# Kernel optimization log

Measured on AMD Instinct MI355X. Metric: run time of the kernel, lower is better.

Reference implementation:

```python
import jax, jax.numpy as jnp
import numpy as np

N_NODES = 100000
N_EDGES = 1600000
N_GRAPHS = 64
NEG_SLOPE = 0.2


def gat_conv(x, W, att_src, att_dst, bias, edge_index, n_nodes, heads, out_ch, concat):
    """PyG-style GATConv (eval mode, self loops already included in edge_index)."""
    h = (x @ W).reshape(n_nodes, heads, out_ch)            # [N, H, C]
    a_src = jnp.einsum('nhc,hc->nh', h, att_src)           # [N, H]
    a_dst = jnp.einsum('nhc,hc->nh', h, att_dst)           # [N, H]
    src, dst = edge_index[0], edge_index[1]
    e = jax.nn.leaky_relu(a_src[src] + a_dst[dst], NEG_SLOPE)   # [E, H]
    # segment softmax over incoming edges of each destination node
    m = jax.ops.segment_max(e, dst, num_segments=n_nodes)      # [N, H]
    ex = jnp.exp(e - m[dst])
    denom = jax.ops.segment_sum(ex, dst, num_segments=n_nodes) # [N, H]
    alpha = ex / denom[dst]                                     # [E, H]
    msg = h[src] * alpha[:, :, None]                            # [E, H, C]
    out = jax.ops.segment_sum(msg, dst, num_segments=n_nodes)   # [N, H, C]
    if concat:
        out = out.reshape(n_nodes, heads * out_ch)
    else:
        out = out.mean(axis=1)
    return out + bias


def setup_inputs() -> dict:
    key = jax.random.key(0)
    ks = jax.random.split(key, 16)
    x = jax.random.normal(ks[0], (N_NODES, 1), dtype=jnp.float32)
    edge_index = jax.random.randint(ks[1], (2, N_EDGES), 0, N_NODES, dtype=jnp.int64)
    batch = jnp.sort(jax.random.randint(ks[2], (N_NODES,), 0, N_GRAPHS, dtype=jnp.int64))
    def glorot(k, shape):
        fan = (shape[0] + shape[-1])
        return jax.random.uniform(k, shape, jnp.float32, -1.0, 1.0) * np.sqrt(6.0 / fan)
    # layer 1: in=1, heads=8, out=8, concat
    W1 = glorot(ks[3], (1, 64))
    att_src1 = glorot(ks[4], (8, 8))
    att_dst1 = glorot(ks[5], (8, 8))
    b1 = jnp.zeros((64,), jnp.float32)
    # layer 2: in=64, heads=8, out=16, mean
    W2 = glorot(ks[6], (64, 128))
    att_src2 = glorot(ks[7], (8, 16))
    att_dst2 = glorot(ks[8], (8, 16))
    b2 = jnp.zeros((16,), jnp.float32)
    # fc 16 -> 4
    Wfc = glorot(ks[9], (16, 4))
    bfc = jnp.zeros((4,), jnp.float32)
    return dict(x=x, W1=W1, att_src1=att_src1, att_dst1=att_dst1, b1=b1,
                W2=W2, att_src2=att_src2, att_dst2=att_dst2, b2=b2,
                Wfc=Wfc, bfc=bfc, edge_index=edge_index, batch=batch)


def reference(x, W1, att_src1, att_dst1, b1, W2, att_src2, att_dst2, b2, Wfc, bfc, edge_index, batch):
    n = x.shape[0]
    # PyG GATConv default add_self_loops=True
    loops = jnp.arange(n, dtype=edge_index.dtype)
    ei = jnp.concatenate([edge_index, jnp.stack([loops, loops])], axis=1)
    h = gat_conv(x, W1, att_src1, att_dst1, b1, ei, n, heads=8, out_ch=8, concat=True)
    h = jax.nn.elu(h)
    # F.dropout(training=False) and attention dropout are no-ops in eval mode
    h = gat_conv(h, W2, att_src2, att_dst2, b2, ei, n, heads=8, out_ch=16, concat=False)
    # global mean pool over graphs
    sums = jax.ops.segment_sum(h, batch, num_segments=N_GRAPHS)          # [G, 16]
    cnts = jax.ops.segment_sum(jnp.ones((n,), h.dtype), batch, num_segments=N_GRAPHS)
    pooled = sums / jnp.maximum(cnts, 1.0)[:, None]
    return pooled @ Wfc + bfc                                            # [G, 4]
```

## Files before the change

### kernel.cpp

```cpp
#include <hip/hip_runtime.h>
#include <hip/hip_fp16.h>

#define N_NODES  100000
#define N_EDGES  1600000
#define N_GRAPHS 64

#define BINSH  8
#define NBIN   392
#define BINCAP 5120
#define EPB    4096

typedef _Float16 half8 __attribute__((ext_vector_type(8)));
typedef float float4v __attribute__((ext_vector_type(4)));

__device__ __forceinline__ float lrelu(float v) { return v > 0.f ? v : 0.2f * v; }
__device__ __forceinline__ float elu_f(float v) { return v > 0.f ? v : __expf(v) - 1.f; }

__global__ __launch_bounds__(1024) void k_binA(
    const int* __restrict__ src, const int* __restrict__ dst,
    const int* __restrict__ batch, int* __restrict__ gbin_cursor,
    int* __restrict__ cnt, int* __restrict__ binned) {
    __shared__ int hist[NBIN], lexcl[NBIN], runbase[NBIN], lcur[NBIN];
    __shared__ int wpart[16];
    __shared__ int gh[N_GRAPHS];
    __shared__ int2 stage[EPB];
    int t = threadIdx.x;
    int e0 = blockIdx.x * EPB;
    for (int b = t; b < NBIN; b += 1024) hist[b] = 0;
    if (t < N_GRAPHS) gh[t] = 0;
    __syncthreads();
    int nid = blockIdx.x * 1024 + t;
    if (nid < N_NODES) atomicAdd(&gh[batch[nid]], 1);
    int e = 4 * t;
    int4 dv = make_int4(0, 0, 0, 0), sv = make_int4(0, 0, 0, 0);
    bool full = (e0 + e + 3 < N_EDGES);
    if (full) {
        dv = *(const int4*)(dst + e0 + e);
        sv = *(const int4*)(src + e0 + e);
        atomicAdd(&hist[dv.x >> BINSH], 1);
        atomicAdd(&hist[dv.y >> BINSH], 1);
        atomicAdd(&hist[dv.z >> BINSH], 1);
        atomicAdd(&hist[dv.w >> BINSH], 1);
    } else {
        for (int k = 0; k < 4; ++k)
            if (e0 + e + k < N_EDGES) atomicAdd(&hist[dst[e0 + e + k] >> BINSH], 1);
    }
    __syncthreads();
    int v = (t < NBIN) ? hist[t] : 0;
    int x = v;
#pragma unroll
    for (int d = 1; d < 64; d <<= 1) {
        int y = __shfl_up(x, d, 64);
        if ((t & 63) >= d) x += y;
    }
    if ((t & 63) == 63) wpart[t >> 6] = x;
    __syncthreads();
    if (t == 0) {
        int a = 0;
        for (int w = 0; w < 16; ++w) { int q = wpart[w]; wpart[w] = a; a += q; }
    }
    __syncthreads();
    int excl = x - v + wpart[t >> 6];
    if (t < NBIN) { lexcl[t] = excl; lcur[t] = excl; }
    __syncthreads();
    if (t < NBIN && v > 0) runbase[t] = atomicAdd(&gbin_cursor[t], v);
    if (t < N_GRAPHS && gh[t]) atomicAdd(&cnt[t], gh[t]);
    __syncthreads();
    if (full) {
        int p, b_;
        b_ = dv.x >> BINSH; p = atomicAdd(&lcur[b_], 1);
        stage[p] = make_int2(((dv.x & 255) << 17) | sv.x, b_);
        b_ = dv.y >> BINSH; p = atomicAdd(&lcur[b_], 1);
        stage[p] = make_int2(((dv.y & 255) << 17) | sv.y, b_);
        b_ = dv.z >> BINSH; p = atomicAdd(&lcur[b_], 1);
        stage[p] = make_int2(((dv.z & 255) << 17) | sv.z, b_);
        b_ = dv.w >> BINSH; p = atomicAdd(&lcur[b_], 1);
        stage[p] = make_int2(((dv.w & 255) << 17) | sv.w, b_);
    } else {
        for (int k = 0; k < 4; ++k) {
            if (e0 + e + k < N_EDGES) {
                int d = dst[e0 + e + k];
                int b_ = d >> BINSH;
                int p = atomicAdd(&lcur[b_], 1);
                stage[p] = make_int2(((d & 255) << 17) | src[e0 + e + k], b_);
            }
        }
    }
    __syncthreads();
    int m = N_EDGES - e0;
    if (m > EPB) m = EPB;
    for (int i = 4 * t; i < 4 * t + 4 && i < m; ++i) {
        int2 pr = stage[i];
        int b_ = pr.y;
        binned[(size_t)b_ * BINCAP + runbase[b_] + (i - lexcl[b_])] = pr.x;
    }
}

__global__ __launch_bounds__(1024) void k_megaB(
    const int* __restrict__ binned, const int* __restrict__ gbin_cursor,
    int* __restrict__ off, int* __restrict__ csr,
    const float* __restrict__ x, const float* __restrict__ W1,
    const float* __restrict__ as1, const float* __restrict__ ad1,
    const float* __restrict__ b1, const float* __restrict__ W2,
    const float* __restrict__ as2, const float* __restrict__ ad2,
    __half2* __restrict__ h2p, float2* __restrict__ ap, float2* __restrict__ dp) {
    __shared__ int hist[256], lstart[256];
    __shared__ int wpart[4];
    __shared__ int s_ebase;
    __shared__ float s1l[256 * 8];
    __shared__ float smWs[512], smWd[512];
    __shared__ float smW1[64], smB1[64];
    __shared__ float ws8s[8], wd8s[8];
    __shared__ _Float16 smWT[128 * 72];
    __shared__ _Float16 smA[256 * 72];
    int b = blockIdx.x, t = threadIdx.x;
    int count = gbin_cursor[b];
    int node0 = b << BINSH;
    const int* my = binned + (size_t)b * BINCAP;

    if (t == 0) s_ebase = 0;
    if (t < 256) hist[t] = 0;
    for (int idx = t; idx < 8192; idx += 1024) {
        int c = idx >> 6, k = idx & 63;
        smWT[c * 72 + k] = (_Float16)W2[k * 128 + c];
    }
    {
        int tt = t & 511;
        int k = tt >> 3, h = tt & 7;
        const float* att = (t < 512) ? as2 : ad2;
        float acc = 0.f;
        for (int c = 0; c < 16; ++c)
            acc += W2[k * 128 + h * 16 + c] * att[h * 16 + c];
        if (t < 512) smWs[k * 8 + h] = acc; else smWd[k * 8 + h] = acc;
    }
    if (t < 64) { smW1[t] = W1[t]; smB1[t] = b1[t]; }
    if (t >= 64 && t < 72) {
        int h = t - 64;
        float s = 0.f, d = 0.f;
        for (int c = 0; c < 8; ++c) {
            float w = W1[h * 8 + c];
            s += w * as1[h * 8 + c];
            d += w * ad1[h * 8 + c];
        }
        ws8s[h] = s;
        wd8s[h] = d;
    }
    __syncthreads();

    if (t < b) atomicAdd(&s_ebase, gbin_cursor[t]);
    for (int i = t; i < count; i += 1024) atomicAdd(&hist[my[i] >> 17], 1);
    __syncthreads();

    int v = (t < 256) ? hist[t] : 0;
    int xx = v;
#pragma unroll
    for (int d = 1; d < 64; d <<= 1) {
        int y = __shfl_up(xx, d, 64);
        if ((t & 63) >= d) xx += y;
    }
    if (t < 256 && (t & 63) == 63) wpart[t >> 6] = xx;
    __syncthreads();
    if (t == 0) {
        int a = 0;
        for (int w = 0; w < 4; ++w) { int q = wpart[w]; wpart[w] = a; a += q; }
    }
    __syncthreads();
    int ebase = s_ebase;
    int excl = xx - v + ((t < 256) ? wpart[t >> 6] : 0);
    if (t < 256) {
        int n = node0 + t;
        if (n < N_NODES) off[n] = ebase + excl;
        lstart[t] = excl;
        hist[t] = excl;
    }
    if (b == 0 && t == 0) off[N_NODES] = N_EDGES;
    __syncthreads();

    for (int i = t; i < count; i += 1024) {
        int pr = my[i];
        int p = atomicAdd(&hist[pr >> 17], 1);
        csr[ebase + p] = pr & 0x1FFFF;
    }
    __syncthreads();

    {
        int nl = t >> 2, c = t & 3;
        int n = node0 + nl;
        float ws[8], wd[8];
#pragma unroll
        for (int h = 0; h < 8; ++h) { ws[h] = ws8s[h]; wd[h] = wd8s[h]; }
        float xn = (n < N_NODES) ? x[n] : 0.f;
        float num[8], den[8];
#pragma unroll
        for (int h = 0; h < 8; ++h) { num[h] = 0.f; den[h] = 0.f; }
        if (c == 0 && n < N_NODES) {
#pragma unroll
            for (int h = 0; h < 8; ++h) {
                float w = __expf(lrelu(xn * ws[h] + xn * wd[h]));
                den[h] = w;
                num[h] = w * xn;
            }
        }
        int st = lstart[nl], en = hist[nl];
        for (int j = st + c; j < en; j += 4) {
            int s = csr[ebase + j];
            float xs = x[s];
#pragma unroll
            for (int h = 0; h < 8; ++h) {
                float w = __expf(lrelu(xs * ws[h] + xn * wd[h]));
                den[h] += w;
                num[h] += w * xs;
            }
        }
#pragma unroll
        for (int d = 1; d < 4; d <<= 1) {
#pragma unroll
            for (int h = 0; h < 8; ++h) {
                num[h] += __shfl_xor(num[h], d, 64);
                den[h] += __shfl_xor(den[h], d, 64);
            }
        }
        if (c == 0) {
#pragma unroll
            for (int h = 0; h < 8; ++h)
                s1l[nl * 8 + h] = (n < N_NODES) ? num[h] / den[h] : 0.f;
        }
    }
    __syncthreads();

    {
        int nl = t >> 2, j = t & 3;
        int n = node0 + nl;
        if (n < N_NODES) {
            float pSA = 0.f, pSB = 0.f, pDA = 0.f, pDB = 0.f;
#pragma unroll 8
            for (int k = 0; k < 64; ++k) {
                float h1a = elu_f(s1l[nl * 8 + (k >> 3)] * smW1[k] + smB1[k]);
                pSA += h1a * smWs[k * 8 + j];
                pSB += h1a * smWs[k * 8 + j + 4];
                pDA += h1a * smWd[k * 8 + j];
                pDB += h1a * smWd[k * 8 + j + 4];
            }
            ap[n * 4 + j] = make_float2(pSA, pSB);
            dp[n * 4 + j] = make_float2(pDA, pDB);
        }
    }
    for (int i = t; i < 256 * 64; i += 1024) {
        int m = i >> 6, k = i & 63;
        smA[m * 72 + k] = (_Float16)elu_f(s1l[m * 8 + (k >> 3)] * smW1[k] + smB1[k]);
    }
    __syncthreads();

    {
        int wave = t >> 6, lane = t & 63;
        int quad = lane >> 4, m15 = lane & 15;
        half8 a0 = *reinterpret_cast<const half8*>(&smA[(wave * 16 + m15) * 72 + quad * 8]);
        half8 a1 = *reinterpret_cast<const half8*>(&smA[(wave * 16 + m15) * 72 + 32 + quad * 8]);
        float4v acc[8];
#pragma unroll
        for (int tl = 0; tl < 8; ++tl) {
            half8 b0 = *reinterpret_cast<const half8*>(&smWT[(tl * 16 + m15) * 72 + quad * 8]);
            half8 b1v = *reinterpret_cast<const half8*>(&smWT[(tl * 16 + m15) * 72 + 32 + quad * 8]);
            float4v c = {0.f, 0.f, 0.f, 0.f};
            c = __builtin_amdgcn_mfma_f32_16x16x32_f16(a0, b0, c, 0, 0, 0);
            c = __builtin_amdgcn_mfma_f32_16x16x32_f16(a1, b1v, c, 0, 0, 0);
            acc[tl] = c;
        }
#pragma unroll
        for (int tl = 0; tl < 4; ++tl) {
#pragma unroll
            for (int reg = 0; reg < 4; ++reg) {
                int n = node0 + wave * 16 + quad * 4 + reg;
                if (n < N_NODES)
                    h2p[n * 64 + tl * 16 + m15] =
                        __floats2half2_rn(acc[tl][reg], acc[tl + 4][reg]);
            }
        }
    }
}

__global__ __launch_bounds__(256, 8) void k_layer2(
    const __half2* __restrict__ h2p, const float2* __restrict__ ap,
    const float2* __restrict__ dp, const int* __restrict__ off,
    const int* __restrict__ csr, const int* __restrict__ batch,
    float* __restrict__ pool) {
    __shared__ float smv[4][16];
    __shared__ int smg[4];
    const float* apf = (const float*)ap;
    const float* dpf = (const float*)dp;
    int t = threadIdx.x;
    int wid = t >> 6, l = t & 63;
    int n = blockIdx.x * 4 + wid;
    int hA = l >> 4;
    int hh = l & 7;
    int j8 = l >> 3;
    int fidx = 2 * (hh & 3) + (hh >> 2);
    float dn = dpf[n * 8 + fidx];

    float2 ad = dp[n * 4 + hA];
    float2 an = ap[n * 4 + hA];
    float wA = __expf(lrelu(an.x + ad.x));
    float wB = __expf(lrelu(an.y + ad.y));
    float2 hn = __half22float2(h2p[n * 64 + l]);
    float accA = wA * hn.x, accB = wB * hn.y;
    float denTA = wA, denTB = wB;
    float wsum = 0.f;

    int b = off[n];
    int deg = off[n + 1] - b;
    for (int base = 0; base < deg; base += 64) {
        int rem = deg - base;
        if (rem > 64) rem = 64;
        int sl = (l < rem) ? csr[b + base + l] : 0;
        int g = 0;
        for (; g + 8 <= rem; g += 8) {
            int sg = __shfl(sl, g + j8, 64);
            float w = __expf(lrelu(apf[sg * 8 + fidx] + dn));
            wsum += w;
#pragma unroll
            for (int j2 = 0; j2 < 8; ++j2) {
                int s = __builtin_amdgcn_readlane(sl, g + j2);
                float wa = __shfl(w, j2 * 8 + hA, 64);
                float wb = __shfl(w, j2 * 8 + hA + 4, 64);
                float2 gg = __half22float2(h2p[s * 64 + l]);
                accA = fmaf(wa, gg.x, accA);
                accB = fmaf(wb, gg.y, accB);
            }
        }
        if (g < rem) {
            int cnt2 = rem - g;
            int jj = (j8 < cnt2) ? j8 : 0;
            int sg = __shfl(sl, g + jj, 64);
            float w = (j8 < cnt2) ? __expf(lrelu(apf[sg * 8 + fidx] + dn)) : 0.f;
            wsum += w;
            for (int j2 = 0; j2 < cnt2; ++j2) {
                int s = __builtin_amdgcn_readlane(sl, g + j2);
                float wa = __shfl(w, j2 * 8 + hA, 64);
                float wb = __shfl(w, j2 * 8 + hA + 4, 64);
                float2 gg = __half22float2(h2p[s * 64 + l]);
                accA = fmaf(wa, gg.x, accA);
                accB = fmaf(wb, gg.y, accB);
            }
        }
    }
    wsum += __shfl_xor(wsum, 8, 64);
    wsum += __shfl_xor(wsum, 16, 64);
    wsum += __shfl_xor(wsum, 32, 64);
    float denA = denTA + __shfl(wsum, hA, 64);
    float denB = denTB + __shfl(wsum, hA + 4, 64);

    float v = accA / denA + accB / denB;
    v += __shfl_xor(v, 16, 64);
    v += __shfl_xor(v, 32, 64);
    v *= 0.125f;
    if (l < 16) smv[wid][l] = v;
    if (l == 0) smg[wid] = batch[n];
    __syncthreads();
    if (t < 64) {
        int w = t >> 4, c = t & 15;
        int g = smg[w];
        bool leader = true;
        for (int w2 = 0; w2 < w; ++w2)
            if (smg[w2] == g) { leader = false; break; }
        if (leader) {
            float s = smv[w][c];
            for (int w2 = w + 1; w2 < 4; ++w2)
                if (smg[w2] == g) s += smv[w2][c];
            atomicAdd(&pool[g * 16 + c], s);
        }
    }
}

__global__ void k_final(const float* __restrict__ pool, const int* __restrict__ cnt,
                        const float* __restrict__ b2, const float* __restrict__ Wfc,
                        const float* __restrict__ bfc, float* __restrict__ out) {
    int t = threadIdx.x;
    int g = t >> 2, k = t & 3;
    float c = (float)(cnt[g] > 0 ? cnt[g] : 1);
    float acc = bfc[k];
#pragma unroll
    for (int ci = 0; ci < 16; ++ci)
        acc += (pool[g * 16 + ci] / c + b2[ci]) * Wfc[ci * 4 + k];
    out[g * 4 + k] = acc;
}

extern "C" void kernel_launch(void* const* d_in, const int* in_sizes, int n_in,
                              void* d_out, int out_size, void* d_ws, size_t ws_size,
                              hipStream_t stream) {
    const float* x   = (const float*)d_in[0];
    const float* W1  = (const float*)d_in[1];
    const float* as1 = (const float*)d_in[2];
    const float* ad1 = (const float*)d_in[3];
    const float* b1  = (const float*)d_in[4];
    const float* W2  = (const float*)d_in[5];
    const float* as2 = (const float*)d_in[6];
    const float* ad2 = (const float*)d_in[7];
    const float* b2  = (const float*)d_in[8];
    const float* Wfc = (const float*)d_in[9];
    const float* bfc = (const float*)d_in[10];
    const int* ei    = (const int*)d_in[11];
    const int* batch = (const int*)d_in[12];
    const int* srcv  = ei;
    const int* dstv  = ei + N_EDGES;

    char* ws = (char*)d_ws;
    size_t o = 0;
    auto alloc = [&](size_t bytes) {
        void* p = ws + o;
        o += (bytes + 255) & ~(size_t)255;
        return p;
    };
    int*    cnt     = (int*)alloc(64 * 4);
    float*  pool    = (float*)alloc(64 * 16 * 4);
    int*    gbin    = (int*)alloc(NBIN * 4);
    size_t  zbytes  = o;
    int*    off     = (int*)alloc((size_t)(N_NODES + 1) * 4);
    int*    csr     = (int*)alloc((size_t)N_EDGES * 4);
    float2* ap      = (float2*)alloc((size_t)N_NODES * 4 * 8);
    float2* dp      = (float2*)alloc((size_t)N_NODES * 4 * 8);
    int*    binned  = (int*)alloc((size_t)NBIN * BINCAP * 4);
    __half2* h2p    = (__half2*)alloc((size_t)N_NODES * 64 * 4);

    hipMemsetAsync(d_ws, 0, zbytes, stream);

    int nbA = (N_EDGES + EPB - 1) / EPB;

    k_binA<<<nbA, 1024, 0, stream>>>(srcv, dstv, batch, gbin, cnt, binned);
    k_megaB<<<NBIN, 1024, 0, stream>>>(binned, gbin, off, csr,
                                       x, W1, as1, ad1, b1, W2, as2, ad2,
                                       h2p, ap, dp);
    k_layer2<<<N_NODES / 4, 256, 0, stream>>>(h2p, ap, dp, off, csr, batch, pool);
    k_final<<<1, 256, 0, stream>>>(pool, cnt, b2, Wfc, bfc, (float*)d_out);
}
```

Measured before the change: 263.8 us.

## Precompute normalized layer-2 attention weights in a separate kernel

Adds a k_wgt kernel that computes the per-edge softmax weights for layer 2, normalizes them by the per-node denominator, and stores them as fp16 in a padded per-node edge array. It also stores the self-loop weights. k_layer2 then reads these weights as half8 vectors instead of computing exp and running shuffles inline, and the final division goes away. The cost is an extra launch, a second pass over csr and the gathered attention scores, about 28 MB of extra fp16 weight traffic, and fp16 rounding of the attention weights.

```diff
diff --git a/kernel.cpp b/kernel.cpp
--- a/kernel.cpp
+++ b/kernel.cpp
@@ -279,77 +279,85 @@
     }
 }
 
+__global__ __launch_bounds__(256, 8) void k_wgt(
+    const float* __restrict__ apf, const float* __restrict__ dpf,
+    const int* __restrict__ off, const int* __restrict__ csr,
+    _Float16* __restrict__ awgt, _Float16* __restrict__ aself) {
+    int t = threadIdx.x;
+    int wid = t >> 6, l = t & 63;
+    int n = blockIdx.x * 4 + wid;
+    int j8 = l >> 3, hh = l & 7;
+    int fidx = 2 * (hh & 3) + (hh >> 2);
+    float dn = dpf[n * 8 + fidx];
+    float wself = __expf(lrelu(apf[n * 8 + fidx] + dn));
+    int b = off[n];
+    int deg = off[n + 1] - b;
+    int pb = b + 8 * n;
+    float wsum = 0.f;
+    for (int k = 0; k < deg; k += 8) {
+        int idx = k + j8;
+        float w = 0.f;
+        if (idx < deg) {
+            int sg = csr[b + idx];
+            w = __expf(lrelu(apf[sg * 8 + fidx] + dn));
+        }
+        wsum += w;
+    }
+    wsum += __shfl_xor(wsum, 8, 64);
+    wsum += __shfl_xor(wsum, 16, 64);
+    wsum += __shfl_xor(wsum, 32, 64);
+    float inv = 1.f / (wself + wsum);
+    if (l < 8) aself[n * 8 + hh] = (_Float16)(wself * inv);
+    for (int k = 0; k < deg; k += 8) {
+        int idx = k + j8;
+        float w = 0.f;
+        if (idx < deg) {
+            int sg = csr[b + idx];
+            w = __expf(lrelu(apf[sg * 8 + fidx] + dn));
+        }
+        awgt[(size_t)(pb + k) * 8 + hh * 8 + j8] = (_Float16)(w * inv);
+    }
+}
+
 __global__ __launch_bounds__(256, 8) void k_layer2(
-    const __half2* __restrict__ h2p, const float2* __restrict__ ap,
-    const float2* __restrict__ dp, const int* __restrict__ off,
+    const __half2* __restrict__ h2p, const _Float16* __restrict__ awgt,
+    const _Float16* __restrict__ aself, const int* __restrict__ off,
     const int* __restrict__ csr, const int* __restrict__ batch,
     float* __restrict__ pool) {
     __shared__ float smv[4][16];
     __shared__ int smg[4];
-    const float* apf = (const float*)ap;
-    const float* dpf = (const float*)dp;
     int t = threadIdx.x;
     int wid = t >> 6, l = t & 63;
     int n = blockIdx.x * 4 + wid;
     int hA = l >> 4;
-    int hh = l & 7;
-    int j8 = l >> 3;
-    int fidx = 2 * (hh & 3) + (hh >> 2);
-    float dn = dpf[n * 8 + fidx];
-
-    float2 ad = dp[n * 4 + hA];
-    float2 an = ap[n * 4 + hA];
-    float wA = __expf(lrelu(an.x + ad.x));
-    float wB = __expf(lrelu(an.y + ad.y));
-    float2 hn = __half22float2(h2p[n * 64 + l]);
-    float accA = wA * hn.x, accB = wB * hn.y;
-    float denTA = wA, denTB = wB;
-    float wsum = 0.f;
+
+    float aSA = (float)aself[n * 8 + hA];
+    float aSB = (float)aself[n * 8 + hA + 4];
+    float2 hf = __half22float2(h2p[(size_t)n * 64 + l]);
+    float acc0 = aSA * hf.x;
+    float acc1 = aSB * hf.y;
 
     int b = off[n];
     int deg = off[n + 1] - b;
+    int pb = b + 8 * n;
     for (int base = 0; base < deg; base += 64) {
         int rem = deg - base;
         if (rem > 64) rem = 64;
         int sl = (l < rem) ? csr[b + base + l] : 0;
-        int g = 0;
-        for (; g + 8 <= rem; g += 8) {
-            int sg = __shfl(sl, g + j8, 64);
-            float w = __expf(lrelu(apf[sg * 8 + fidx] + dn));
-            wsum += w;
-#pragma unroll
-            for (int j2 = 0; j2 < 8; ++j2) {
-                int s = __builtin_amdgcn_readlane(sl, g + j2);
-                float wa = __shfl(w, j2 * 8 + hA, 64);
-                float wb = __shfl(w, j2 * 8 + hA + 4, 64);
-                float2 gg = __half22float2(h2p[s * 64 + l]);
-                accA = fmaf(wa, gg.x, accA);
-                accB = fmaf(wb, gg.y, accB);
-            }
-        }
-        if (g < rem) {
-            int cnt2 = rem - g;
-            int jj = (j8 < cnt2) ? j8 : 0;
-            int sg = __shfl(sl, g + jj, 64);
-            float w = (j8 < cnt2) ? __expf(lrelu(apf[sg * 8 + fidx] + dn)) : 0.f;
-            wsum += w;
-            for (int j2 = 0; j2 < cnt2; ++j2) {
-                int s = __builtin_amdgcn_readlane(sl, g + j2);
-                float wa = __shfl(w, j2 * 8 + hA, 64);
-                float wb = __shfl(w, j2 * 8 + hA + 4, 64);
-                float2 gg = __half22float2(h2p[s * 64 + l]);
-                accA = fmaf(wa, gg.x, accA);
-                accB = fmaf(wb, gg.y, accB);
-            }
-        }
-    }
-    wsum += __shfl_xor(wsum, 8, 64);
-    wsum += __shfl_xor(wsum, 16, 64);
-    wsum += __shfl_xor(wsum, 32, 64);
-    float denA = denTA + __shfl(wsum, hA, 64);
-    float denB = denTB + __shfl(wsum, hA + 4, 64);
-
-    float v = accA / denA + accB / denB;
+        for (int g = 0; g < rem; g += 8) {
+            const _Float16* grp = &awgt[(size_t)(pb + base + g) * 8];
+            half8 aA = *reinterpret_cast<const half8*>(grp + hA * 8);
+            half8 aB = *reinterpret_cast<const half8*>(grp + (hA + 4) * 8);
+#pragma unroll
+            for (int e = 0; e < 8; ++e) {
+                int s = __builtin_amdgcn_readlane(sl, g + e);
+                float2 gf = __half22float2(h2p[(size_t)s * 64 + l]);
+                acc0 = fmaf((float)aA[e], gf.x, acc0);
+                acc1 = fmaf((float)aB[e], gf.y, acc1);
+            }
+        }
+    }
+    float v = acc0 + acc1;
     v += __shfl_xor(v, 16, 64);
     v += __shfl_xor(v, 32, 64);
     v *= 0.125f;
@@ -420,6 +428,8 @@
     float2* dp      = (float2*)alloc((size_t)N_NODES * 4 * 8);
     int*    binned  = (int*)alloc((size_t)NBIN * BINCAP * 4);
     __half2* h2p    = (__half2*)alloc((size_t)N_NODES * 64 * 4);
+    _Float16* awgt  = (_Float16*)alloc((size_t)(N_EDGES + 8 * N_NODES + 8) * 8 * 2);
+    _Float16* aself = (_Float16*)alloc((size_t)N_NODES * 8 * 2);
 
     hipMemsetAsync(d_ws, 0, zbytes, stream);
 
@@ -429,6 +439,9 @@
     k_megaB<<<NBIN, 1024, 0, stream>>>(binned, gbin, off, csr,
                                        x, W1, as1, ad1, b1, W2, as2, ad2,
                                        h2p, ap, dp);
-    k_layer2<<<N_NODES / 4, 256, 0, stream>>>(h2p, ap, dp, off, csr, batch, pool);
+    k_wgt<<<N_NODES / 4, 256, 0, stream>>>((const float*)ap, (const float*)dp,
+                                           off, csr, awgt, aself);
+    k_layer2<<<N_NODES / 4, 256, 0, stream>>>(h2p, awgt, aself, off, csr,
+                                              batch, pool);
     k_final<<<1, 256, 0, stream>>>(pool, cnt, b2, Wfc, bfc, (float*)d_out);
 }
```

Result: slower. 297.4 us (+12.7%).

## Split layer-2 projection GEMM out of megaB into separate 64-node kernel

Applied to the files above, without the earlier changes.

Moves the elu, feature projection and MFMA GEMM for layer 2 out of the 392-block megaB kernel into a new k_gemm kernel that processes 64 nodes per 256-thread block. The layer-1 aggregate is written to a global buffer s1g and read back. The goal is to cut megaB's large shared-memory footprint and give the GEMM phase many more blocks for better occupancy. In exchange it adds one kernel launch, an extra global round trip of 3.2 MB, and a per-block reload of W2 and its attention projections. Several h2p indices are also widened to size_t.

```diff
diff --git a/kernel.cpp b/kernel.cpp
--- a/kernel.cpp
+++ b/kernel.cpp
@@ -101,18 +101,12 @@
     int* __restrict__ off, int* __restrict__ csr,
     const float* __restrict__ x, const float* __restrict__ W1,
     const float* __restrict__ as1, const float* __restrict__ ad1,
-    const float* __restrict__ b1, const float* __restrict__ W2,
-    const float* __restrict__ as2, const float* __restrict__ ad2,
-    __half2* __restrict__ h2p, float2* __restrict__ ap, float2* __restrict__ dp) {
+    float* __restrict__ s1g) {
     __shared__ int hist[256], lstart[256];
     __shared__ int wpart[4];
     __shared__ int s_ebase;
     __shared__ float s1l[256 * 8];
-    __shared__ float smWs[512], smWd[512];
-    __shared__ float smW1[64], smB1[64];
     __shared__ float ws8s[8], wd8s[8];
-    __shared__ _Float16 smWT[128 * 72];
-    __shared__ _Float16 smA[256 * 72];
     int b = blockIdx.x, t = threadIdx.x;
     int count = gbin_cursor[b];
     int node0 = b << BINSH;
@@ -120,20 +114,6 @@
 
     if (t == 0) s_ebase = 0;
     if (t < 256) hist[t] = 0;
-    for (int idx = t; idx < 8192; idx += 1024) {
-        int c = idx >> 6, k = idx & 63;
-        smWT[c * 72 + k] = (_Float16)W2[k * 128 + c];
-    }
-    {
-        int tt = t & 511;
-        int k = tt >> 3, h = tt & 7;
-        const float* att = (t < 512) ? as2 : ad2;
-        float acc = 0.f;
-        for (int c = 0; c < 16; ++c)
-            acc += W2[k * 128 + h * 16 + c] * att[h * 16 + c];
-        if (t < 512) smWs[k * 8 + h] = acc; else smWd[k * 8 + h] = acc;
-    }
-    if (t < 64) { smW1[t] = W1[t]; smB1[t] = b1[t]; }
     if (t >= 64 && t < 72) {
         int h = t - 64;
         float s = 0.f, d = 0.f;
@@ -227,6 +207,43 @@
         }
     }
     __syncthreads();
+    for (int i = t; i < 2048; i += 1024) {
+        int n = node0 + (i >> 3);
+        if (n < N_NODES) s1g[(size_t)node0 * 8 + i] = s1l[i];
+    }
+}
+
+__global__ __launch_bounds__(256, 4) void k_gemm(
+    const float* __restrict__ s1g, const float* __restrict__ W1,
+    const float* __restrict__ b1, const float* __restrict__ W2,
+    const float* __restrict__ as2, const float* __restrict__ ad2,
+    __half2* __restrict__ h2p, float2* __restrict__ ap, float2* __restrict__ dp) {
+    __shared__ _Float16 smWT[128 * 72];
+    __shared__ _Float16 smA[64 * 72];
+    __shared__ float smWs[512], smWd[512];
+    __shared__ float smW1[64], smB1[64];
+    __shared__ float smS1[512];
+    int t = threadIdx.x;
+    int node0 = blockIdx.x * 64;
+    for (int idx = t; idx < 8192; idx += 256) {
+        int c = idx >> 6, k = idx & 63;
+        smWT[c * 72 + k] = (_Float16)W2[k * 128 + c];
+    }
+    for (int tt = t; tt < 1024; tt += 256) {
+        int inner = tt & 511;
+        int k = inner >> 3, h = inner & 7;
+        const float* att = (tt < 512) ? as2 : ad2;
+        float acc = 0.f;
+        for (int c = 0; c < 16; ++c)
+            acc += W2[k * 128 + h * 16 + c] * att[h * 16 + c];
+        if (tt < 512) smWs[k * 8 + h] = acc; else smWd[k * 8 + h] = acc;
+    }
+    if (t < 64) { smW1[t] = W1[t]; smB1[t] = b1[t]; }
+    for (int i = t; i < 512; i += 256) {
+        int n = node0 + (i >> 3);
+        smS1[i] = (n < N_NODES) ? s1g[(size_t)n * 8 + (i & 7)] : 0.f;
+    }
+    __syncthreads();
 
     {
         int nl = t >> 2, j = t & 3;
@@ -235,7 +252,7 @@
             float pSA = 0.f, pSB = 0.f, pDA = 0.f, pDB = 0.f;
 #pragma unroll 8
             for (int k = 0; k < 64; ++k) {
-                float h1a = elu_f(s1l[nl * 8 + (k >> 3)] * smW1[k] + smB1[k]);
+                float h1a = elu_f(smS1[nl * 8 + (k >> 3)] * smW1[k] + smB1[k]);
                 pSA += h1a * smWs[k * 8 + j];
                 pSB += h1a * smWs[k * 8 + j + 4];
                 pDA += h1a * smWd[k * 8 + j];
@@ -245,9 +262,9 @@
             dp[n * 4 + j] = make_float2(pDA, pDB);
         }
     }
-    for (int i = t; i < 256 * 64; i += 1024) {
+    for (int i = t; i < 64 * 64; i += 256) {
         int m = i >> 6, k = i & 63;
-        smA[m * 72 + k] = (_Float16)elu_f(s1l[m * 8 + (k >> 3)] * smW1[k] + smB1[k]);
+        smA[m * 72 + k] = (_Float16)elu_f(smS1[m * 8 + (k >> 3)] * smW1[k] + smB1[k]);
     }
     __syncthreads();
 
@@ -272,7 +289,7 @@
             for (int reg = 0; reg < 4; ++reg) {
                 int n = node0 + wave * 16 + quad * 4 + reg;
                 if (n < N_NODES)
-                    h2p[n * 64 + tl * 16 + m15] =
+                    h2p[(size_t)n * 64 + tl * 16 + m15] =
                         __floats2half2_rn(acc[tl][reg], acc[tl + 4][reg]);
             }
         }
@@ -301,7 +318,7 @@
     float2 an = ap[n * 4 + hA];
     float wA = __expf(lrelu(an.x + ad.x));
     float wB = __expf(lrelu(an.y + ad.y));
-    float2 hn = __half22float2(h2p[n * 64 + l]);
+    float2 hn = __half22float2(h2p[(size_t)n * 64 + l]);
     float accA = wA * hn.x, accB = wB * hn.y;
     float denTA = wA, denTB = wB;
     float wsum = 0.f;
@@ -322,7 +339,7 @@
                 int s = __builtin_amdgcn_readlane(sl, g + j2);
                 float wa = __shfl(w, j2 * 8 + hA, 64);
                 float wb = __shfl(w, j2 * 8 + hA + 4, 64);
-                float2 gg = __half22float2(h2p[s * 64 + l]);
+                float2 gg = __half22float2(h2p[(size_t)s * 64 + l]);
                 accA = fmaf(wa, gg.x, accA);
                 accB = fmaf(wb, gg.y, accB);
             }
@@ -337,7 +354,7 @@
                 int s = __builtin_amdgcn_readlane(sl, g + j2);
                 float wa = __shfl(w, j2 * 8 + hA, 64);
                 float wb = __shfl(w, j2 * 8 + hA + 4, 64);
-                float2 gg = __half22float2(h2p[s * 64 + l]);
+                float2 gg = __half22float2(h2p[(size_t)s * 64 + l]);
                 accA = fmaf(wa, gg.x, accA);
                 accB = fmaf(wb, gg.y, accB);
             }
@@ -420,15 +437,17 @@
     float2* dp      = (float2*)alloc((size_t)N_NODES * 4 * 8);
     int*    binned  = (int*)alloc((size_t)NBIN * BINCAP * 4);
     __half2* h2p    = (__half2*)alloc((size_t)N_NODES * 64 * 4);
+    float*  s1g     = (float*)alloc((size_t)N_NODES * 8 * 4);
 
     hipMemsetAsync(d_ws, 0, zbytes, stream);
 
     int nbA = (N_EDGES + EPB - 1) / EPB;
+    int nbG = (N_NODES + 63) / 64;
 
     k_binA<<<nbA, 1024, 0, stream>>>(srcv, dstv, batch, gbin, cnt, binned);
     k_megaB<<<NBIN, 1024, 0, stream>>>(binned, gbin, off, csr,
-                                       x, W1, as1, ad1, b1, W2, as2, ad2,
-                                       h2p, ap, dp);
+                                       x, W1, as1, ad1, s1g);
+    k_gemm<<<nbG, 256, 0, stream>>>(s1g, W1, b1, W2, as2, ad2, h2p, ap, dp);
     k_layer2<<<N_NODES / 4, 256, 0, stream>>>(h2p, ap, dp, off, csr, batch, pool);
     k_final<<<1, 256, 0, stream>>>(pool, cnt, b2, Wfc, bfc, (float*)d_out);
 }
```

Result: slower. 281.0 us (+6.5%).
